# Kernel optimization log

Measured on AMD Instinct MI355X. Metric: run time of the kernel, lower is better.

Reference implementation:

```python
import jax, jax.numpy as jnp
import numpy as np
from jax.ops import segment_sum

N_NODES = 50000
N_EDGES = 800000
IN_DIM, HID_DIM, OUT_DIM = 128, 256, 128


def _glorot(key, shape):
    lim = np.sqrt(6.0 / (shape[0] + shape[1]))
    return jax.random.uniform(key, shape, jnp.float32, -lim, lim)


def setup_inputs() -> dict:
    key = jax.random.key(0)
    ks = jax.random.split(key, 4)
    x = jax.random.normal(ks[0], (N_NODES, IN_DIM), jnp.float32)
    edge_index = jax.random.randint(ks[1], (2, N_EDGES), 0, N_NODES, jnp.int64)
    W1 = _glorot(ks[2], (IN_DIM, HID_DIM))
    b1 = jnp.zeros((HID_DIM,), jnp.float32)
    W2 = _glorot(ks[3], (HID_DIM, OUT_DIM))
    b2 = jnp.zeros((OUT_DIM,), jnp.float32)
    return {"x": x, "edge_index": edge_index, "W1": W1, "b1": b1, "W2": W2, "b2": b2}


def gcn_conv(x, W, b, src, dst, n_nodes):
    # PyG GCNConv: x' = D^{-1/2} (A + I) D^{-1/2} (x W) + b
    h = x @ W  # [N, F_out]
    deg = segment_sum(jnp.ones_like(src, dtype=h.dtype), dst, num_segments=n_nodes) + 1.0  # +1 self loop
    dinv = jax.lax.rsqrt(deg)  # [N]
    norm = dinv[src] * dinv[dst]  # per-edge norm [E]
    msg = h[src] * norm[:, None]  # [E, F_out]
    agg = segment_sum(msg, dst, num_segments=n_nodes)
    agg = agg + h * (dinv * dinv)[:, None]  # self-loop term: norm_ii = dinv_i^2
    return agg + b


def reference(x, edge_index, W1, b1, W2, b2):
    src, dst = edge_index[0], edge_index[1]
    h = gcn_conv(x, W1, b1, src, dst, N_NODES)
    h = jax.nn.relu(h)
    out = gcn_conv(h, W2, b2, src, dst, N_NODES)
    return out
```

## Files before the change

### kernel.cpp

```cpp
#include <hip/hip_runtime.h>

#define N_NODES 50000
#define N_EDGES 800000
#define IN_DIM  128
#define HID_DIM 256
#define OUT_DIM 128
#define BUCKET_CAP 64
#define NCOARSE 196
#define COARSE_CAP 4800
#define CHUNK 4000
#define NBLK1 200

typedef __attribute__((ext_vector_type(8))) short short8;
typedef __attribute__((ext_vector_type(4))) float f32x4;

__device__ inline ushort f2b(float f) {
    union { float f; unsigned u; } v; v.f = f;
    return (ushort)((v.u + 0x7FFFu + ((v.u >> 16) & 1u)) >> 16);
}
__device__ inline float b2f(ushort h) {
    union { unsigned u; float f; } v; v.u = ((unsigned)h) << 16;
    return v.f;
}
__device__ inline float2 u2f2(unsigned u) {
    float2 r; r.x = b2f((ushort)(u & 0xFFFFu)); r.y = b2f((ushort)(u >> 16)); return r;
}
__device__ inline void fma2(float2& a, const float2 v, float n) {
    a.x += v.x * n; a.y += v.y * n;
}


__global__ void conv_x_kernel(const float* __restrict__ x, ushort* __restrict__ xb,
                              int* __restrict__ bincnt) {
    int i = blockIdx.x * blockDim.x + threadIdx.x;
    if (i < NCOARSE) bincnt[i] = 0;
    float4 v = ((const float4*)x)[i];
    ushort4 o; o.x = f2b(v.x); o.y = f2b(v.y); o.z = f2b(v.z); o.w = f2b(v.w);
    ((ushort4*)xb)[i] = o;
}

__global__ void conv_w_kernel(const float* __restrict__ W1, const float* __restrict__ W2,
                              ushort* __restrict__ w1t, ushort* __restrict__ w2t) {
    int i = blockIdx.x * blockDim.x + threadIdx.x;
    if (i < 32768) {
        int n = i >> 7, k = i & 127;
        w1t[i] = f2b(W1[k * HID_DIM + n]);
    } else {
        int j = i - 32768;
        int n = j >> 8, k = j & 255;
        w2t[j] = f2b(W2[k * OUT_DIM + n]);
    }
}


__global__ __launch_bounds__(256) void binpass1_kernel(const int* __restrict__ src,
                                                       const int* __restrict__ dst,
                                                       int* __restrict__ bincnt,
                                                       int* __restrict__ binbuf) {
    __shared__ int vals[CHUNK];
    __shared__ ushort lpos[CHUNK];
    __shared__ unsigned char lbin[CHUNK];
    __shared__ int hist[NCOARSE];
    __shared__ int base[NCOARSE];
    const int t = threadIdx.x;
    const int e0 = blockIdx.x * CHUNK;
    for (int i = t; i < NCOARSE; i += 256) hist[i] = 0;
    __syncthreads();
    for (int i = t; i < CHUNK; i += 256) {
        int s = src[e0 + i], d = dst[e0 + i];
        int b = d >> 8;
        vals[i] = (s << 8) | (d & 255);
        lbin[i] = (unsigned char)b;
        lpos[i] = (ushort)atomicAdd(&hist[b], 1);
    }
    __syncthreads();
    for (int i = t; i < NCOARSE; i += 256) base[i] = atomicAdd(&bincnt[i], hist[i]);
    __syncthreads();
    for (int i = t; i < CHUNK; i += 256) {
        int b = lbin[i];
        int p = base[b] + lpos[i];
        if (p < COARSE_CAP) binbuf[b * COARSE_CAP + p] = vals[i];
    }
}

__global__ __launch_bounds__(256) void binpass2_kernel(const int* __restrict__ bincnt,
                                                       const int* __restrict__ binbuf,
                                                       int* __restrict__ cnt,
                                                       float* __restrict__ dinv,
                                                       int* __restrict__ bucket) {
    __shared__ int lcnt[256];
    __shared__ int lbuck[256 * BUCKET_CAP];
    const int bin = blockIdx.x;
    const int t = threadIdx.x;
    lcnt[t] = 0;
    __syncthreads();
    int m = bincnt[bin];
    if (m > COARSE_CAP) m = COARSE_CAP;
    const int* bb = binbuf + (size_t)bin * COARSE_CAP;
    for (int j = t; j < m; j += 256) {
        int v = bb[j];
        int dl = v & 255;
        int pos = atomicAdd(&lcnt[dl], 1);
        if (pos < BUCKET_CAP) lbuck[dl * BUCKET_CAP + pos] = v >> 8;
    }
    __syncthreads();
    const int node0 = bin * 256;
    int node = node0 + t;
    if (node < N_NODES) {
        int c = lcnt[t] > BUCKET_CAP ? BUCKET_CAP : lcnt[t];
        cnt[node] = c;
        dinv[node] = rsqrtf((float)c + 1.0f);
    }
    int nvalid = N_NODES - node0; if (nvalid > 256) nvalid = 256;
    if (nvalid <= 0) return;
    int total4 = (nvalid * BUCKET_CAP) >> 2;
    int4* d4 = (int4*)(bucket + (size_t)node0 * BUCKET_CAP);
    const int4* s4 = (const int4*)lbuck;
    for (int j = t; j < total4; j += 256) d4[j] = s4[j];
}


__global__ __launch_bounds__(256) void gather0_kernel(const int* __restrict__ cnt,
                                                      const int* __restrict__ bucket,
                                                      const float* __restrict__ dinv,
                                                      const ushort* __restrict__ xb,
                                                      ushort* __restrict__ aggxb) {
    const int w = blockIdx.x * 4 + (threadIdx.x >> 6);
    const int lane = threadIdx.x & 63;
    const int n = cnt[w];
    const float dd = dinv[w];
    int sv = 0; float nv = 0.f;
    if (lane < n) { sv = bucket[w * BUCKET_CAP + lane]; nv = dinv[sv] * dd; }

    float2 self = u2f2(((const unsigned*)(xb + (size_t)w * IN_DIM))[lane]);
    float sd = dd * dd;
    float2 acc[8];
    acc[0] = {self.x * sd, self.y * sd};
#pragma unroll
    for (int j = 1; j < 8; ++j) acc[j] = {0.f, 0.f};

    const int nr = (n + 7) & ~7;
    for (int i = 0; i < nr; i += 8) {
        int s[8]; float nm[8]; unsigned u[8];
#pragma unroll
        for (int j = 0; j < 8; ++j) { s[j] = __shfl(sv, i + j); nm[j] = __shfl(nv, i + j); }
#pragma unroll
        for (int j = 0; j < 8; ++j) u[j] = ((const unsigned*)(xb + (size_t)s[j] * IN_DIM))[lane];
#pragma unroll
        for (int j = 0; j < 8; ++j) fma2(acc[j], u2f2(u[j]), nm[j]);
    }
#pragma unroll
    for (int j = 1; j < 8; ++j) { acc[0].x += acc[j].x; acc[0].y += acc[j].y; }
    unsigned o = (unsigned)f2b(acc[0].x) | ((unsigned)f2b(acc[0].y) << 16);
    ((unsigned*)(aggxb + (size_t)w * IN_DIM))[lane] = o;
}


__global__ __launch_bounds__(256) void gemm1_mfma(const ushort* __restrict__ aggxb,
                                                  const ushort* __restrict__ w1t,
                                                  const float* __restrict__ b1,
                                                  ushort* __restrict__ Hb) {
    const int row0 = blockIdx.x * 16;
    const int wv = threadIdx.x >> 6;
    const int lane = threadIdx.x & 63;
    const int l15 = lane & 15, q = lane >> 4;
    f32x4 acc[4] = {{0.f, 0.f, 0.f, 0.f}, {0.f, 0.f, 0.f, 0.f},
                    {0.f, 0.f, 0.f, 0.f}, {0.f, 0.f, 0.f, 0.f}};
    const ushort* abase = aggxb + (size_t)(row0 + l15) * IN_DIM + q * 8;
#pragma unroll
    for (int kb = 0; kb < 4; ++kb) {
        short8 a = *(const short8*)(abase + kb * 32);
#pragma unroll
        for (int t = 0; t < 4; ++t) {
            int col = wv * 64 + t * 16 + l15;
            short8 b = *(const short8*)(w1t + (size_t)col * IN_DIM + kb * 32 + q * 8);
            acc[t] = __builtin_amdgcn_mfma_f32_16x16x32_bf16(a, b, acc[t], 0, 0, 0);
        }
    }
#pragma unroll
    for (int t = 0; t < 4; ++t) {
        int col = wv * 64 + t * 16 + l15;
        float bias = b1[col];
#pragma unroll
        for (int r = 0; r < 4; ++r) {
            int row = row0 + q * 4 + r;
            float v = acc[t][r] + bias;
            Hb[(size_t)row * HID_DIM + col] = f2b(v > 0.f ? v : 0.f);
        }
    }
}


__global__ __launch_bounds__(256) void gemm2_mfma(const ushort* __restrict__ Hb,
                                                  const ushort* __restrict__ w2t,
                                                  ushort* __restrict__ h2b) {
    const int row0 = blockIdx.x * 16;
    const int wv = threadIdx.x >> 6;
    const int lane = threadIdx.x & 63;
    const int l15 = lane & 15, q = lane >> 4;
    f32x4 acc[2] = {{0.f, 0.f, 0.f, 0.f}, {0.f, 0.f, 0.f, 0.f}};
    const ushort* abase = Hb + (size_t)(row0 + l15) * HID_DIM + q * 8;
#pragma unroll
    for (int kb = 0; kb < 8; ++kb) {
        short8 a = *(const short8*)(abase + kb * 32);
#pragma unroll
        for (int t = 0; t < 2; ++t) {
            int col = wv * 32 + t * 16 + l15;
            short8 b = *(const short8*)(w2t + (size_t)col * HID_DIM + kb * 32 + q * 8);
            acc[t] = __builtin_amdgcn_mfma_f32_16x16x32_bf16(a, b, acc[t], 0, 0, 0);
        }
    }
#pragma unroll
    for (int t = 0; t < 2; ++t) {
        int col = wv * 32 + t * 16 + l15;
#pragma unroll
        for (int r = 0; r < 4; ++r) {
            int row = row0 + q * 4 + r;
            h2b[(size_t)row * OUT_DIM + col] = f2b(acc[t][r]);
        }
    }
}


__global__ __launch_bounds__(256) void gather2_kernel(const int* __restrict__ cnt,
                                                      const int* __restrict__ bucket,
                                                      const float* __restrict__ dinv,
                                                      const ushort* __restrict__ h2b,
                                                      const float* __restrict__ b2,
                                                      float* __restrict__ out) {
    const int w = blockIdx.x * 4 + (threadIdx.x >> 6);
    const int lane = threadIdx.x & 63;
    const int n = cnt[w];
    const float dd = dinv[w];
    int sv = 0; float nv = 0.f;
    if (lane < n) { sv = bucket[w * BUCKET_CAP + lane]; nv = dinv[sv] * dd; }

    float2 bb = ((const float2*)b2)[lane];
    float2 self = u2f2(((const unsigned*)(h2b + (size_t)w * OUT_DIM))[lane]);
    float sd = dd * dd;
    float2 acc[8];
    acc[0] = {self.x * sd + bb.x, self.y * sd + bb.y};
#pragma unroll
    for (int j = 1; j < 8; ++j) acc[j] = {0.f, 0.f};

    const int nr = (n + 7) & ~7;
    for (int i = 0; i < nr; i += 8) {
        int s[8]; float nm[8]; unsigned u[8];
#pragma unroll
        for (int j = 0; j < 8; ++j) { s[j] = __shfl(sv, i + j); nm[j] = __shfl(nv, i + j); }
#pragma unroll
        for (int j = 0; j < 8; ++j) u[j] = ((const unsigned*)(h2b + (size_t)s[j] * OUT_DIM))[lane];
#pragma unroll
        for (int j = 0; j < 8; ++j) fma2(acc[j], u2f2(u[j]), nm[j]);
    }
#pragma unroll
    for (int j = 1; j < 8; ++j) { acc[0].x += acc[j].x; acc[0].y += acc[j].y; }
    ((float2*)(out + (size_t)w * OUT_DIM))[lane] = acc[0];
}

extern "C" void kernel_launch(void* const* d_in, const int* in_sizes, int n_in,
                              void* d_out, int out_size, void* d_ws, size_t ws_size,
                              hipStream_t stream) {
    const float* x  = (const float*)d_in[0];
    const int*   ei = (const int*)d_in[1];
    const float* W1 = (const float*)d_in[2];
    const float* b1 = (const float*)d_in[3];
    const float* W2 = (const float*)d_in[4];
    const float* b2 = (const float*)d_in[5];
    float* out = (float*)d_out;

    const int* src = ei;
    const int* dst = ei + N_EDGES;

    char* ws = (char*)d_ws;
    int*    bincnt = (int*)(ws);
    int*    cnt    = (int*)(ws + 1024);
    float*  dinv   = (float*)(ws + 201024);
    int*    bucket = (int*)(ws + 401024);
    int*    binbuf = (int*)(ws + 13201024);
    ushort* xb     = (ushort*)(ws + 16964224);
    ushort* aggxb  = (ushort*)(ws + 29764224);
    ushort* w1t    = (ushort*)(ws + 42564224);
    ushort* w2t    = (ushort*)(ws + 42629760);
    ushort* Hb     = (ushort*)(ws + 42695296);
    ushort* h2b    = (ushort*)(ws + 68295296);

    conv_x_kernel<<<(N_NODES * IN_DIM / 4) / 256, 256, 0, stream>>>(x, xb, bincnt);
    conv_w_kernel<<<65536 / 256, 256, 0, stream>>>(W1, W2, w1t, w2t);
    binpass1_kernel<<<NBLK1, 256, 0, stream>>>(src, dst, bincnt, binbuf);
    binpass2_kernel<<<NCOARSE, 256, 0, stream>>>(bincnt, binbuf, cnt, dinv, bucket);

    gather0_kernel<<<N_NODES / 4, 256, 0, stream>>>(cnt, bucket, dinv, xb, aggxb);
    gemm1_mfma<<<N_NODES / 16, 256, 0, stream>>>(aggxb, w1t, b1, Hb);

    gemm2_mfma<<<N_NODES / 16, 256, 0, stream>>>(Hb, w2t, h2b);
    gather2_kernel<<<N_NODES / 4, 256, 0, stream>>>(cnt, bucket, dinv, h2b, b2, out);
}
```

Before: 243.7 us.

## Fuse prep kernels, drop global atomics in binning, fuse gather0 into gemm1

Merges the x/W conversion kernels and the first binning pass into one launch. Binning now writes fixed per-block segments with per-block counts instead of claiming space with global atomics, so bincnt no longer needs zeroing. The layer-1 aggregation now runs inside the first GEMM kernel and stages the aggregated rows in padded shared memory instead of writing aggxb to global memory. This removes two launches, one global round trip and the atomic contention. In exchange, binpass2 scans a sparse 200x64 segment grid and each per-block segment is capped at 64 edges, which could drop edges for skewed inputs.

Result: slower. 251.3 us (+3.1%).

```diff
diff --git a/kernel.cpp b/kernel.cpp
--- a/kernel.cpp
+++ b/kernel.cpp
@@ -7,9 +7,10 @@
 #define OUT_DIM 128
 #define BUCKET_CAP 64
 #define NCOARSE 196
-#define COARSE_CAP 4800
 #define CHUNK 4000
 #define NBLK1 200
+#define SEGCAP 64
+#define AXLD 136
 
 typedef __attribute__((ext_vector_type(8))) short short8;
 typedef __attribute__((ext_vector_type(4))) float f32x4;
@@ -30,78 +31,86 @@
 }
 
 
-__global__ void conv_x_kernel(const float* __restrict__ x, ushort* __restrict__ xb,
-                              int* __restrict__ bincnt) {
-    int i = blockIdx.x * blockDim.x + threadIdx.x;
-    if (i < NCOARSE) bincnt[i] = 0;
-    float4 v = ((const float4*)x)[i];
-    ushort4 o; o.x = f2b(v.x); o.y = f2b(v.y); o.z = f2b(v.z); o.w = f2b(v.w);
-    ((ushort4*)xb)[i] = o;
-}
-
-__global__ void conv_w_kernel(const float* __restrict__ W1, const float* __restrict__ W2,
-                              ushort* __restrict__ w1t, ushort* __restrict__ w2t) {
-    int i = blockIdx.x * blockDim.x + threadIdx.x;
-    if (i < 32768) {
-        int n = i >> 7, k = i & 127;
-        w1t[i] = f2b(W1[k * HID_DIM + n]);
-    } else {
-        int j = i - 32768;
-        int n = j >> 8, k = j & 255;
-        w2t[j] = f2b(W2[k * OUT_DIM + n]);
-    }
-}
-
-
-__global__ __launch_bounds__(256) void binpass1_kernel(const int* __restrict__ src,
-                                                       const int* __restrict__ dst,
-                                                       int* __restrict__ bincnt,
-                                                       int* __restrict__ binbuf) {
+__global__ __launch_bounds__(256) void prep_kernel(const float* __restrict__ x,
+                                                   const float* __restrict__ W1,
+                                                   const float* __restrict__ W2,
+                                                   const int* __restrict__ src,
+                                                   const int* __restrict__ dst,
+                                                   ushort* __restrict__ xb,
+                                                   ushort* __restrict__ w1t,
+                                                   ushort* __restrict__ w2t,
+                                                   int* __restrict__ bcnt,
+                                                   int* __restrict__ binbuf) {
     __shared__ int vals[CHUNK];
     __shared__ ushort lpos[CHUNK];
     __shared__ unsigned char lbin[CHUNK];
     __shared__ int hist[NCOARSE];
-    __shared__ int base[NCOARSE];
+    const int b = blockIdx.x;
     const int t = threadIdx.x;
-    const int e0 = blockIdx.x * CHUNK;
-    for (int i = t; i < NCOARSE; i += 256) hist[i] = 0;
-    __syncthreads();
-    for (int i = t; i < CHUNK; i += 256) {
-        int s = src[e0 + i], d = dst[e0 + i];
-        int b = d >> 8;
-        vals[i] = (s << 8) | (d & 255);
-        lbin[i] = (unsigned char)b;
-        lpos[i] = (ushort)atomicAdd(&hist[b], 1);
-    }
-    __syncthreads();
-    for (int i = t; i < NCOARSE; i += 256) base[i] = atomicAdd(&bincnt[i], hist[i]);
-    __syncthreads();
-    for (int i = t; i < CHUNK; i += 256) {
-        int b = lbin[i];
-        int p = base[b] + lpos[i];
-        if (p < COARSE_CAP) binbuf[b * COARSE_CAP + p] = vals[i];
-    }
-}
-
-__global__ __launch_bounds__(256) void binpass2_kernel(const int* __restrict__ bincnt,
+    if (b < 6250) {
+        int i = b * 256 + t;
+        float4 v = ((const float4*)x)[i];
+        ushort4 o; o.x = f2b(v.x); o.y = f2b(v.y); o.z = f2b(v.z); o.w = f2b(v.w);
+        ((ushort4*)xb)[i] = o;
+    } else if (b < 6506) {
+        int i = (b - 6250) * 256 + t;
+        if (i < 32768) {
+            int n = i >> 7, k = i & 127;
+            w1t[i] = f2b(W1[k * HID_DIM + n]);
+        } else {
+            int j = i - 32768;
+            int n = j >> 8, k = j & 255;
+            w2t[j] = f2b(W2[k * OUT_DIM + n]);
+        }
+    } else {
+        const int blk = b - 6506;
+        const int e0 = blk * CHUNK;
+        for (int i = t; i < NCOARSE; i += 256) hist[i] = 0;
+        __syncthreads();
+        for (int i = t; i < CHUNK; i += 256) {
+            int s = src[e0 + i], d = dst[e0 + i];
+            int bin = d >> 8;
+            vals[i] = (s << 8) | (d & 255);
+            lbin[i] = (unsigned char)bin;
+            lpos[i] = (ushort)atomicAdd(&hist[bin], 1);
+        }
+        __syncthreads();
+        for (int i = t; i < NCOARSE; i += 256) {
+            int h = hist[i]; if (h > SEGCAP) h = SEGCAP;
+            bcnt[i * NBLK1 + blk] = h;
+        }
+        for (int i = t; i < CHUNK; i += 256) {
+            int bin = lbin[i];
+            int p = lpos[i];
+            if (p < SEGCAP) binbuf[((size_t)bin * NBLK1 + blk) * SEGCAP + p] = vals[i];
+        }
+    }
+}
+
+
+__global__ __launch_bounds__(256) void binpass2_kernel(const int* __restrict__ bcnt,
                                                        const int* __restrict__ binbuf,
                                                        int* __restrict__ cnt,
                                                        float* __restrict__ dinv,
                                                        int* __restrict__ bucket) {
     __shared__ int lcnt[256];
+    __shared__ int lm[NBLK1];
     __shared__ int lbuck[256 * BUCKET_CAP];
     const int bin = blockIdx.x;
     const int t = threadIdx.x;
     lcnt[t] = 0;
+    if (t < NBLK1) lm[t] = bcnt[bin * NBLK1 + t];
     __syncthreads();
-    int m = bincnt[bin];
-    if (m > COARSE_CAP) m = COARSE_CAP;
-    const int* bb = binbuf + (size_t)bin * COARSE_CAP;
-    for (int j = t; j < m; j += 256) {
-        int v = bb[j];
-        int dl = v & 255;
-        int pos = atomicAdd(&lcnt[dl], 1);
-        if (pos < BUCKET_CAP) lbuck[dl * BUCKET_CAP + pos] = v >> 8;
+    const int* bb = binbuf + (size_t)bin * NBLK1 * SEGCAP;
+    for (int f = t; f < NBLK1 * SEGCAP; f += 256) {
+        int blk = f >> 6;
+        int sl = f & 63;
+        if (sl < lm[blk]) {
+            int v = bb[f];
+            int dl = v & 255;
+            int pos = atomicAdd(&lcnt[dl], 1);
+            if (pos < BUCKET_CAP) lbuck[dl * BUCKET_CAP + pos] = v >> 8;
+        }
     }
     __syncthreads();
     const int node0 = bin * 256;
@@ -120,61 +129,60 @@
 }
 
 
-__global__ __launch_bounds__(256) void gather0_kernel(const int* __restrict__ cnt,
-                                                      const int* __restrict__ bucket,
-                                                      const float* __restrict__ dinv,
-                                                      const ushort* __restrict__ xb,
-                                                      ushort* __restrict__ aggxb) {
-    const int w = blockIdx.x * 4 + (threadIdx.x >> 6);
-    const int lane = threadIdx.x & 63;
-    const int n = cnt[w];
-    const float dd = dinv[w];
-    int sv = 0; float nv = 0.f;
-    if (lane < n) { sv = bucket[w * BUCKET_CAP + lane]; nv = dinv[sv] * dd; }
-
-    float2 self = u2f2(((const unsigned*)(xb + (size_t)w * IN_DIM))[lane]);
-    float sd = dd * dd;
-    float2 acc[8];
-    acc[0] = {self.x * sd, self.y * sd};
-#pragma unroll
-    for (int j = 1; j < 8; ++j) acc[j] = {0.f, 0.f};
-
-    const int nr = (n + 7) & ~7;
-    for (int i = 0; i < nr; i += 8) {
-        int s[8]; float nm[8]; unsigned u[8];
-#pragma unroll
-        for (int j = 0; j < 8; ++j) { s[j] = __shfl(sv, i + j); nm[j] = __shfl(nv, i + j); }
-#pragma unroll
-        for (int j = 0; j < 8; ++j) u[j] = ((const unsigned*)(xb + (size_t)s[j] * IN_DIM))[lane];
-#pragma unroll
-        for (int j = 0; j < 8; ++j) fma2(acc[j], u2f2(u[j]), nm[j]);
-    }
-#pragma unroll
-    for (int j = 1; j < 8; ++j) { acc[0].x += acc[j].x; acc[0].y += acc[j].y; }
-    unsigned o = (unsigned)f2b(acc[0].x) | ((unsigned)f2b(acc[0].y) << 16);
-    ((unsigned*)(aggxb + (size_t)w * IN_DIM))[lane] = o;
-}
-
-
-__global__ __launch_bounds__(256) void gemm1_mfma(const ushort* __restrict__ aggxb,
+__global__ __launch_bounds__(256) void gg1_kernel(const int* __restrict__ cnt,
+                                                  const int* __restrict__ bucket,
+                                                  const float* __restrict__ dinv,
+                                                  const ushort* __restrict__ xb,
                                                   const ushort* __restrict__ w1t,
                                                   const float* __restrict__ b1,
                                                   ushort* __restrict__ Hb) {
+    __shared__ ushort axs[16 * AXLD];
     const int row0 = blockIdx.x * 16;
     const int wv = threadIdx.x >> 6;
     const int lane = threadIdx.x & 63;
+
+    for (int j = 0; j < 4; ++j) {
+        const int lr = wv * 4 + j;
+        const int node = row0 + lr;
+        const int n = cnt[node];
+        const float dd = dinv[node];
+        int sv = 0; float nv = 0.f;
+        if (lane < n) { sv = bucket[node * BUCKET_CAP + lane]; nv = dinv[sv] * dd; }
+        float2 self = u2f2(((const unsigned*)(xb + (size_t)node * IN_DIM))[lane]);
+        float sd = dd * dd;
+        float2 acc[8];
+        acc[0] = {self.x * sd, self.y * sd};
+#pragma unroll
+        for (int k = 1; k < 8; ++k) acc[k] = {0.f, 0.f};
+        const int nr = (n + 7) & ~7;
+        for (int i = 0; i < nr; i += 8) {
+            int s[8]; float nm[8]; unsigned u[8];
+#pragma unroll
+            for (int k = 0; k < 8; ++k) { s[k] = __shfl(sv, i + k); nm[k] = __shfl(nv, i + k); }
+#pragma unroll
+            for (int k = 0; k < 8; ++k) u[k] = ((const unsigned*)(xb + (size_t)s[k] * IN_DIM))[lane];
+#pragma unroll
+            for (int k = 0; k < 8; ++k) fma2(acc[k], u2f2(u[k]), nm[k]);
+        }
+#pragma unroll
+        for (int k = 1; k < 8; ++k) { acc[0].x += acc[k].x; acc[0].y += acc[k].y; }
+        unsigned o = (unsigned)f2b(acc[0].x) | ((unsigned)f2b(acc[0].y) << 16);
+        ((unsigned*)(axs + lr * AXLD))[lane] = o;
+    }
+    __syncthreads();
+
     const int l15 = lane & 15, q = lane >> 4;
-    f32x4 acc[4] = {{0.f, 0.f, 0.f, 0.f}, {0.f, 0.f, 0.f, 0.f},
-                    {0.f, 0.f, 0.f, 0.f}, {0.f, 0.f, 0.f, 0.f}};
-    const ushort* abase = aggxb + (size_t)(row0 + l15) * IN_DIM + q * 8;
+    f32x4 acc4[4] = {{0.f, 0.f, 0.f, 0.f}, {0.f, 0.f, 0.f, 0.f},
+                     {0.f, 0.f, 0.f, 0.f}, {0.f, 0.f, 0.f, 0.f}};
+    const ushort* abase = axs + l15 * AXLD + q * 8;
 #pragma unroll
     for (int kb = 0; kb < 4; ++kb) {
         short8 a = *(const short8*)(abase + kb * 32);
 #pragma unroll
         for (int t = 0; t < 4; ++t) {
             int col = wv * 64 + t * 16 + l15;
-            short8 b = *(const short8*)(w1t + (size_t)col * IN_DIM + kb * 32 + q * 8);
-            acc[t] = __builtin_amdgcn_mfma_f32_16x16x32_bf16(a, b, acc[t], 0, 0, 0);
+            short8 bfr = *(const short8*)(w1t + (size_t)col * IN_DIM + kb * 32 + q * 8);
+            acc4[t] = __builtin_amdgcn_mfma_f32_16x16x32_bf16(a, bfr, acc4[t], 0, 0, 0);
         }
     }
 #pragma unroll
@@ -184,7 +192,7 @@
 #pragma unroll
         for (int r = 0; r < 4; ++r) {
             int row = row0 + q * 4 + r;
-            float v = acc[t][r] + bias;
+            float v = acc4[t][r] + bias;
             Hb[(size_t)row * HID_DIM + col] = f2b(v > 0.f ? v : 0.f);
         }
     }
@@ -273,25 +281,21 @@
     const int* dst = ei + N_EDGES;
 
     char* ws = (char*)d_ws;
-    int*    bincnt = (int*)(ws);
-    int*    cnt    = (int*)(ws + 1024);
-    float*  dinv   = (float*)(ws + 201024);
-    int*    bucket = (int*)(ws + 401024);
-    int*    binbuf = (int*)(ws + 13201024);
-    ushort* xb     = (ushort*)(ws + 16964224);
-    ushort* aggxb  = (ushort*)(ws + 29764224);
-    ushort* w1t    = (ushort*)(ws + 42564224);
-    ushort* w2t    = (ushort*)(ws + 42629760);
-    ushort* Hb     = (ushort*)(ws + 42695296);
-    ushort* h2b    = (ushort*)(ws + 68295296);
-
-    conv_x_kernel<<<(N_NODES * IN_DIM / 4) / 256, 256, 0, stream>>>(x, xb, bincnt);
-    conv_w_kernel<<<65536 / 256, 256, 0, stream>>>(W1, W2, w1t, w2t);
-    binpass1_kernel<<<NBLK1, 256, 0, stream>>>(src, dst, bincnt, binbuf);
-    binpass2_kernel<<<NCOARSE, 256, 0, stream>>>(bincnt, binbuf, cnt, dinv, bucket);
-
-    gather0_kernel<<<N_NODES / 4, 256, 0, stream>>>(cnt, bucket, dinv, xb, aggxb);
-    gemm1_mfma<<<N_NODES / 16, 256, 0, stream>>>(aggxb, w1t, b1, Hb);
+    int*    bcnt   = (int*)(ws);
+    int*    cnt    = (int*)(ws + 160000);
+    float*  dinv   = (float*)(ws + 360000);
+    int*    bucket = (int*)(ws + 560000);
+    int*    binbuf = (int*)(ws + 13360000);
+    ushort* xb     = (ushort*)(ws + 23395200);
+    ushort* w1t    = (ushort*)(ws + 36195200);
+    ushort* w2t    = (ushort*)(ws + 36260736);
+    ushort* Hb     = (ushort*)(ws + 36326272);
+    ushort* h2b    = (ushort*)(ws + 61926272);
+
+    prep_kernel<<<6706, 256, 0, stream>>>(x, W1, W2, src, dst, xb, w1t, w2t, bcnt, binbuf);
+    binpass2_kernel<<<NCOARSE, 256, 0, stream>>>(bcnt, binbuf, cnt, dinv, bucket);
+
+    gg1_kernel<<<N_NODES / 16, 256, 0, stream>>>(cnt, bucket, dinv, xb, w1t, b1, Hb);
 
     gemm2_mfma<<<N_NODES / 16, 256, 0, stream>>>(Hb, w2t, h2b);
     gather2_kernel<<<N_NODES / 4, 256, 0, stream>>>(cnt, bucket, dinv, h2b, b2, out);
```
